# Kernel optimization log

Hardware: AMD Instinct MI355X
Metric: run time of the kernel (lower is better)

The kernel has to match this reference:

```python
import jax, jax.numpy as jnp
import numpy as np

N_GRAPHS = 256
BN_EPS = 1e-5

def gcn_conv(x, row, col, W, b, n):
    # PyG GCNConv: add self-loops, symmetric deg^-1/2 normalization, scatter-add at col.
    deg = jnp.zeros((n,), x.dtype).at[col].add(1.0) + 1.0  # +1 for self-loop
    dinv = jax.lax.rsqrt(deg)
    xw = x @ W                                             # [N, H]
    msg = (dinv[row] * dinv[col])[:, None] * xw[row]       # [E, H] gathered messages
    agg = jnp.zeros_like(xw).at[col].add(msg)              # scatter-add to targets
    agg = agg + (dinv * dinv)[:, None] * xw                # self-loop contribution
    return agg + b

def batch_norm(x, gamma, beta):
    # BatchNorm1d over the node dimension (training-mode batch statistics)
    mu = jnp.mean(x, axis=0)
    var = jnp.var(x, axis=0)
    return (x - mu) * jax.lax.rsqrt(var + BN_EPS) * gamma + beta

def setup_inputs():
    key = jax.random.key(0)
    ks = jax.random.split(key, 8)
    N, F, H, C, E = 50000, 128, 128, 3, 1_600_000
    x = jax.random.normal(ks[0], (N, F), jnp.float32)
    edge_index = jax.random.randint(ks[1], (2, E), 0, N)
    batch = jnp.sort(jax.random.randint(ks[2], (N,), 0, N_GRAPHS))
    s = lambda k, sh, fan: jax.random.normal(k, sh, jnp.float32) / np.sqrt(fan).astype(np.float32)
    return {
        "x": x, "edge_index": edge_index, "batch": batch,
        "W1": s(ks[3], (F, H), F), "b1": jnp.zeros((H,), jnp.float32),
        "gamma1": jnp.ones((H,), jnp.float32), "beta1": jnp.zeros((H,), jnp.float32),
        "W2": s(ks[4], (H, H), H), "b2": jnp.zeros((H,), jnp.float32),
        "gamma2": jnp.ones((H,), jnp.float32), "beta2": jnp.zeros((H,), jnp.float32),
        "Wc": s(ks[5], (3 * H, C), 3 * H), "bc": jnp.zeros((C,), jnp.float32),
    }

def reference(x, edge_index, batch, W1, b1, gamma1, beta1, W2, b2, gamma2, beta2, Wc, bc):
    n = x.shape[0]
    row, col = edge_index[0], edge_index[1]
    h = jax.nn.relu(batch_norm(gcn_conv(x, row, col, W1, b1, n), gamma1, beta1))
    # dropout is identity in eval mode
    h = jax.nn.relu(batch_norm(gcn_conv(h, row, col, W2, b2, n), gamma2, beta2))
    cnt = jax.ops.segment_sum(jnp.ones((n,), h.dtype), batch, num_segments=N_GRAPHS)
    hsum = jax.ops.segment_sum(h, batch, num_segments=N_GRAPHS)
    hmean = hsum / jnp.maximum(cnt, 1.0)[:, None]
    hmax = jax.ops.segment_max(h, batch, num_segments=N_GRAPHS)
    hmax = jnp.where(cnt[:, None] > 0, hmax, 0.0)  # guard empty graphs
    g = jnp.concatenate([hmean, hmax, hsum], axis=1)  # [G, 3H]
    return g @ Wc + bc
```

## Files before the change

kernel.cpp:

```cpp
#include <hip/hip_runtime.h>

#define HF 128
#define TILE 128
#define CAP2 6144
#define NFINE_MAX 512
#define SORT_CHUNK 4096
#define BN_EPS 1e-5f

__device__ __forceinline__ unsigned short f2bf(float f) {
    unsigned u = __float_as_uint(f);
    unsigned rounding = 0x7FFF + ((u >> 16) & 1);
    return (unsigned short)((u + rounding) >> 16);
}
__device__ __forceinline__ float bf2f(unsigned short u) {
    return __uint_as_float(((unsigned)u) << 16);
}
__device__ __forceinline__ unsigned packbf(float lo, float hi) {
    return ((unsigned)f2bf(hi) << 16) | (unsigned)f2bf(lo);
}

__global__ __launch_bounds__(256) void bucket_sort(const int* __restrict__ row,
                                                   const int* __restrict__ col,
                                                   unsigned* __restrict__ buckets,
                                                   int* __restrict__ cursor,
                                                   int E, int nfine) {
    __shared__ int hist[NFINE_MAX], lbase[NFINE_MAX], gbase[NFINE_MAX], lofs[NFINE_MAX];
    __shared__ int s[512];
    __shared__ unsigned staged[SORT_CHUNK];
    __shared__ unsigned short sbkt[SORT_CHUNK];
    int t = threadIdx.x;
    for (int i = t; i < NFINE_MAX; i += 256) { hist[i] = 0; lofs[i] = 0; }
    __syncthreads();
    int e0 = blockIdx.x * SORT_CHUNK;
    int n = min(SORT_CHUNK, E - e0);
    for (int i = t; i < n; i += 256) {
        int c = col[e0 + i];
        atomicAdd(&hist[c >> 7], 1);
    }
    __syncthreads();
    s[t] = hist[t];
    s[t + 256] = hist[t + 256];
    for (int o = 1; o < 512; o <<= 1) {
        __syncthreads();
        int idx = (t + 1) * (o << 1) - 1;
        if (idx < 512) s[idx] += s[idx - o];
    }
    __syncthreads();
    if (t == 0) s[511] = 0;
    for (int o = 256; o >= 1; o >>= 1) {
        __syncthreads();
        int idx = (t + 1) * (o << 1) - 1;
        if (idx < 512) { int tmp = s[idx - o]; s[idx - o] = s[idx]; s[idx] += tmp; }
    }
    __syncthreads();
    lbase[t] = s[t];
    lbase[t + 256] = s[t + 256];
    for (int b = t; b < nfine; b += 256) {
        int cnt = hist[b];
        gbase[b] = cnt ? atomicAdd(&cursor[b * 16], cnt) : 0;
    }
    __syncthreads();
    for (int i = t; i < n; i += 256) {
        int c = col[e0 + i];
        int r = row[e0 + i];
        int b = c >> 7;
        int pos = lbase[b] + atomicAdd(&lofs[b], 1);
        staged[pos] = ((unsigned)(c & 127) << 17) | (unsigned)r;
        sbkt[pos] = (unsigned short)b;
    }
    __syncthreads();
    for (int i = t; i < n; i += 256) {
        int b = sbkt[i];
        int pos = gbase[b] + (i - lbase[b]);
        if (pos < CAP2) buckets[(size_t)b * CAP2 + pos] = staged[i];
    }
}

__global__ __launch_bounds__(256) void tile_place2(const unsigned* __restrict__ buckets,
                                                   const int* __restrict__ cursor,
                                                   int* __restrict__ rowptr,
                                                   float* __restrict__ dinv,
                                                   int* __restrict__ srow,
                                                   const int* __restrict__ batch,
                                                   int* __restrict__ gstart,
                                                   int N, int NG, int nfine) {
    int b = blockIdx.x;
    int t = threadIdx.x;
    if (b < 2 && t < 129) {
        int g = b * 129 + t;
        if (g <= NG) {
            int lo = 0, hi = N;
            while (lo < hi) {
                int mid = (lo + hi) >> 1;
                if (batch[mid] < g) lo = mid + 1; else hi = mid;
            }
            gstart[g] = lo;
        }
    }
    __shared__ int h[TILE], loc[TILE], cur[TILE];
    __shared__ int red[256];
    __shared__ int stage[CAP2];
    int part = 0;
    for (int i = t; i < b; i += 256) part += min(cursor[i * 16], CAP2);
    red[t] = part;
    if (t < TILE) h[t] = 0;
    __syncthreads();
    for (int o = 128; o > 0; o >>= 1) {
        if (t < o) red[t] += red[t + o];
        __syncthreads();
    }
    int base = red[0];
    int sz = min(cursor[b * 16], CAP2);
    const unsigned* bk = buckets + (size_t)b * CAP2;
    for (int i = t; i < sz; i += 256) atomicAdd(&h[bk[i] >> 17], 1);
    __syncthreads();
    if (t < TILE) loc[t] = h[t];
    __syncthreads();
    for (int o = 1; o < TILE; o <<= 1) {
        int v = (t < TILE && t >= o) ? loc[t - o] : 0;
        __syncthreads();
        if (t < TILE) loc[t] += v;
        __syncthreads();
    }
    if (t < TILE) {
        int c = b * TILE + t;
        int excl = loc[t] - h[t];
        if (c < N) {
            rowptr[c] = base + excl;
            dinv[c] = rsqrtf((float)h[t] + 1.0f);
        }
        cur[t] = excl;
    }
    if (b == nfine - 1 && t == 0) rowptr[N] = base + sz;
    __syncthreads();
    for (int i = t; i < sz; i += 256) {
        unsigned p = bk[i];
        int pos = atomicAdd(&cur[p >> 17], 1);
        if (pos < CAP2) stage[pos] = (int)(p & 0x1FFFFu);
    }
    __syncthreads();
    for (int i = t; i < sz; i += 256) srow[base + i] = stage[i];
}

__global__ __launch_bounds__(256) void gemm_rt(const float* __restrict__ Xf,
                                               const unsigned short* __restrict__ Xh,
                                               const float* __restrict__ W,
                                               unsigned short* __restrict__ Y,
                                               const float* __restrict__ scale,
                                               const float* __restrict__ shift,
                                               const float* __restrict__ rowscale,
                                               int N, int applyBN) {
    __shared__ float xst[HF][68];
    int t = threadIdx.x;
    int row0 = blockIdx.x * 64;
    {
        int f = t & 127;
        float sc = applyBN ? scale[f] : 1.0f;
        float sh = applyBN ? shift[f] : 0.0f;
        for (int r = (t >> 7); r < 64; r += 2) {
            int rr = row0 + r;
            float v = 0.0f;
            if (rr < N) {
                if (applyBN) {
                    v = bf2f(Xh[(size_t)rr * HF + f]);
                    v = fmaxf(v * sc + sh, 0.0f);
                } else {
                    v = Xf[(size_t)rr * HF + f];
                }
            }
            xst[f][r] = v;
        }
    }
    __syncthreads();
    int cg = t & 31;
    int rg = t >> 5;
    int r0 = rg * 8;
    float acc[8][4] = {};
    const float4* Wv = reinterpret_cast<const float4*>(W);
    #pragma unroll 2
    for (int f = 0; f < HF; ++f) {
        float4 w = Wv[f * 32 + cg];
        float4 x0 = *reinterpret_cast<const float4*>(&xst[f][r0]);
        float4 x1 = *reinterpret_cast<const float4*>(&xst[f][r0 + 4]);
        float xr[8] = {x0.x, x0.y, x0.z, x0.w, x1.x, x1.y, x1.z, x1.w};
        #pragma unroll
        for (int i = 0; i < 8; ++i) {
            acc[i][0] += xr[i] * w.x;
            acc[i][1] += xr[i] * w.y;
            acc[i][2] += xr[i] * w.z;
            acc[i][3] += xr[i] * w.w;
        }
    }
    #pragma unroll
    for (int i = 0; i < 8; ++i) {
        int rr = row0 + r0 + i;
        if (rr < N) {
            float rs = rowscale[rr];
            ushort4 o;
            o.x = f2bf(acc[i][0] * rs);
            o.y = f2bf(acc[i][1] * rs);
            o.z = f2bf(acc[i][2] * rs);
            o.w = f2bf(acc[i][3] * rs);
            *reinterpret_cast<ushort4*>(&Y[(size_t)rr * HF + cg * 4]) = o;
        }
    }
}

__global__ __launch_bounds__(256) void gather_conv(const int* __restrict__ rowptr,
                                                   const int* __restrict__ srow,
                                                   const float* __restrict__ dinv,
                                                   const unsigned short* __restrict__ XW,
                                                   const float* __restrict__ b,
                                                   unsigned short* __restrict__ OUT,
                                                   float* __restrict__ psum,
                                                   float* __restrict__ psq, int N) {
    int blk = blockIdx.x;
    int c = blk * 16 + (threadIdx.x >> 4);
    int j = threadIdx.x & 15;
    bool valid = (c < N);
    const unsigned M = 0xffff0000u;
    float o[8];
    if (valid) {
        int e = rowptr[c], end = rowptr[c + 1];
        float acc[8] = {0.f, 0.f, 0.f, 0.f, 0.f, 0.f, 0.f, 0.f};
        for (; e + 3 < end; e += 4) {
            int r0 = srow[e], r1 = srow[e + 1], r2 = srow[e + 2], r3 = srow[e + 3];
            uint4 u0 = *reinterpret_cast<const uint4*>(XW + (size_t)r0 * HF + j * 8);
            uint4 u1 = *reinterpret_cast<const uint4*>(XW + (size_t)r1 * HF + j * 8);
            uint4 u2 = *reinterpret_cast<const uint4*>(XW + (size_t)r2 * HF + j * 8);
            uint4 u3 = *reinterpret_cast<const uint4*>(XW + (size_t)r3 * HF + j * 8);
            acc[0] += (__uint_as_float(u0.x << 16) + __uint_as_float(u1.x << 16))
                    + (__uint_as_float(u2.x << 16) + __uint_as_float(u3.x << 16));
            acc[1] += (__uint_as_float(u0.x & M) + __uint_as_float(u1.x & M))
                    + (__uint_as_float(u2.x & M) + __uint_as_float(u3.x & M));
            acc[2] += (__uint_as_float(u0.y << 16) + __uint_as_float(u1.y << 16))
                    + (__uint_as_float(u2.y << 16) + __uint_as_float(u3.y << 16));
            acc[3] += (__uint_as_float(u0.y & M) + __uint_as_float(u1.y & M))
                    + (__uint_as_float(u2.y & M) + __uint_as_float(u3.y & M));
            acc[4] += (__uint_as_float(u0.z << 16) + __uint_as_float(u1.z << 16))
                    + (__uint_as_float(u2.z << 16) + __uint_as_float(u3.z << 16));
            acc[5] += (__uint_as_float(u0.z & M) + __uint_as_float(u1.z & M))
                    + (__uint_as_float(u2.z & M) + __uint_as_float(u3.z & M));
            acc[6] += (__uint_as_float(u0.w << 16) + __uint_as_float(u1.w << 16))
                    + (__uint_as_float(u2.w << 16) + __uint_as_float(u3.w << 16));
            acc[7] += (__uint_as_float(u0.w & M) + __uint_as_float(u1.w & M))
                    + (__uint_as_float(u2.w & M) + __uint_as_float(u3.w & M));
        }
        for (; e < end; ++e) {
            int r0 = srow[e];
            uint4 u0 = *reinterpret_cast<const uint4*>(XW + (size_t)r0 * HF + j * 8);
            acc[0] += __uint_as_float(u0.x << 16);
            acc[1] += __uint_as_float(u0.x & M);
            acc[2] += __uint_as_float(u0.y << 16);
            acc[3] += __uint_as_float(u0.y & M);
            acc[4] += __uint_as_float(u0.z << 16);
            acc[5] += __uint_as_float(u0.z & M);
            acc[6] += __uint_as_float(u0.w << 16);
            acc[7] += __uint_as_float(u0.w & M);
        }
        float dc = dinv[c];
        uint4 xv = *reinterpret_cast<const uint4*>(XW + (size_t)c * HF + j * 8);
        acc[0] += __uint_as_float(xv.x << 16);
        acc[1] += __uint_as_float(xv.x & M);
        acc[2] += __uint_as_float(xv.y << 16);
        acc[3] += __uint_as_float(xv.y & M);
        acc[4] += __uint_as_float(xv.z << 16);
        acc[5] += __uint_as_float(xv.z & M);
        acc[6] += __uint_as_float(xv.w << 16);
        acc[7] += __uint_as_float(xv.w & M);
        float4 b0 = *reinterpret_cast<const float4*>(b + j * 8);
        float4 b1 = *reinterpret_cast<const float4*>(b + j * 8 + 4);
        float dcv = dc;
        o[0] = dcv * acc[0] + b0.x;
        o[1] = dcv * acc[1] + b0.y;
        o[2] = dcv * acc[2] + b0.z;
        o[3] = dcv * acc[3] + b0.w;
        o[4] = dcv * acc[4] + b1.x;
        o[5] = dcv * acc[5] + b1.y;
        o[6] = dcv * acc[6] + b1.z;
        o[7] = dcv * acc[7] + b1.w;
        uint4 ov;
        ov.x = packbf(o[0], o[1]);
        ov.y = packbf(o[2], o[3]);
        ov.z = packbf(o[4], o[5]);
        ov.w = packbf(o[6], o[7]);
        *reinterpret_cast<uint4*>(OUT + (size_t)c * HF + j * 8) = ov;
    } else {
        #pragma unroll
        for (int k = 0; k < 8; ++k) o[k] = 0.f;
    }
    __shared__ float sval[16][HF + 4];
    int r = threadIdx.x >> 4;
    *reinterpret_cast<float4*>(&sval[r][j * 8]) = make_float4(o[0], o[1], o[2], o[3]);
    *reinterpret_cast<float4*>(&sval[r][j * 8 + 4]) = make_float4(o[4], o[5], o[6], o[7]);
    __syncthreads();
    if (threadIdx.x < HF) {
        float s = 0.f, sq = 0.f;
        #pragma unroll
        for (int rr = 0; rr < 16; ++rr) {
            float v = sval[rr][threadIdx.x];
            s += v;
            sq += v * v;
        }
        psum[(size_t)blk * HF + threadIdx.x] = s;
        psq[(size_t)blk * HF + threadIdx.x] = sq;
    }
}

__global__ __launch_bounds__(256) void bn_reduce(const float* __restrict__ psum,
                                                 const float* __restrict__ psq,
                                                 const float* __restrict__ gamma,
                                                 const float* __restrict__ beta,
                                                 float* __restrict__ scale,
                                                 float* __restrict__ shift,
                                                 int nblk, int N) {
    int f = blockIdx.x;
    int t = threadIdx.x;
    float s = 0.f, sq = 0.f;
    for (int i = t; i < nblk; i += 256) {
        s += psum[(size_t)i * HF + f];
        sq += psq[(size_t)i * HF + f];
    }
    __shared__ float ls[256], lq[256];
    ls[t] = s; lq[t] = sq;
    __syncthreads();
    for (int o = 128; o > 0; o >>= 1) {
        if (t < o) { ls[t] += ls[t + o]; lq[t] += lq[t + o]; }
        __syncthreads();
    }
    if (t == 0) {
        float invn = 1.0f / (float)N;
        float mu = ls[0] * invn;
        float var = lq[0] * invn - mu * mu;
        float sc = gamma[f] * rsqrtf(var + BN_EPS);
        scale[f] = sc;
        shift[f] = beta[f] - mu * sc;
    }
}

__global__ __launch_bounds__(256) void pool_classify(const unsigned short* __restrict__ Bh,
                                                     const int* __restrict__ gstart,
                                                     const float* __restrict__ scale,
                                                     const float* __restrict__ shift,
                                                     const float* __restrict__ Wc,
                                                     const float* __restrict__ bc,
                                                     float* __restrict__ out) {
    int g = blockIdx.x;
    int t = threadIdx.x & 127;
    int half = threadIdx.x >> 7;
    int s0 = gstart[g], s1 = gstart[g + 1];
    float sc = scale[t], sh = shift[t];
    float sum = 0.f, mx = 0.f;
    for (int n = s0 + half; n < s1; n += 2) {
        float v = fmaxf(bf2f(Bh[(size_t)n * HF + t]) * sc + sh, 0.0f);
        sum += v;
        mx = fmaxf(mx, v);
    }
    __shared__ float shsum[2][HF], shmax[2][HF];
    __shared__ float red[3][HF];
    shsum[half][t] = sum;
    shmax[half][t] = mx;
    __syncthreads();
    if (half == 0) {
        sum += shsum[1][t];
        mx = fmaxf(mx, shmax[1][t]);
        float cntf = (float)(s1 - s0);
        float mean = sum / fmaxf(cntf, 1.0f);
        red[0][t] = mean * Wc[t * 3 + 0] + mx * Wc[(HF + t) * 3 + 0] + sum * Wc[(2 * HF + t) * 3 + 0];
        red[1][t] = mean * Wc[t * 3 + 1] + mx * Wc[(HF + t) * 3 + 1] + sum * Wc[(2 * HF + t) * 3 + 1];
        red[2][t] = mean * Wc[t * 3 + 2] + mx * Wc[(HF + t) * 3 + 2] + sum * Wc[(2 * HF + t) * 3 + 2];
    }
    __syncthreads();
    for (int o = 64; o > 0; o >>= 1) {
        if (half == 0 && t < o) {
            red[0][t] += red[0][t + o];
            red[1][t] += red[1][t + o];
            red[2][t] += red[2][t + o];
        }
        __syncthreads();
    }
    if (threadIdx.x < 3) out[g * 3 + threadIdx.x] = red[threadIdx.x][0] + bc[threadIdx.x];
}

extern "C" void kernel_launch(void* const* d_in, const int* in_sizes, int n_in,
                              void* d_out, int out_size, void* d_ws, size_t ws_size,
                              hipStream_t stream) {
    const float* x    = (const float*)d_in[0];
    const int*   ei   = (const int*)d_in[1];
    const int*   batch= (const int*)d_in[2];
    const float* W1   = (const float*)d_in[3];
    const float* b1   = (const float*)d_in[4];
    const float* g1   = (const float*)d_in[5];
    const float* be1  = (const float*)d_in[6];
    const float* W2   = (const float*)d_in[7];
    const float* b2   = (const float*)d_in[8];
    const float* g2   = (const float*)d_in[9];
    const float* be2  = (const float*)d_in[10];
    const float* Wc   = (const float*)d_in[11];
    const float* bc   = (const float*)d_in[12];
    float* out = (float*)d_out;

    const int N = in_sizes[0] / HF;
    const int E = in_sizes[1] / 2;
    const int NG = 256;
    const int* row = ei;
    const int* col = ei + E;
    const int total = N * HF;
    const int nfine = (N + TILE - 1) / TILE;
    const int nblkGa = (N + 15) / 16;

    char* w = (char*)d_ws;
    size_t off = 0;
    auto alloc = [&](size_t bytes) -> void* {
        void* p = w + off;
        off += (bytes + 255) & ~(size_t)255;
        return p;
    };
    int*            cursor    = (int*)alloc((size_t)nfine * 16 * 4);
    float*          dinv      = (float*)alloc((size_t)N * 4);
    int*            rowptr    = (int*)alloc(((size_t)N + 1) * 4);
    int*            gstart    = (int*)alloc((NG + 1) * 4);
    int*            srow      = (int*)alloc((size_t)E * 4);
    float*          psum      = (float*)alloc((size_t)nblkGa * HF * 4);
    float*          psq       = (float*)alloc((size_t)nblkGa * HF * 4);
    float*          scale     = (float*)alloc(HF * 4);
    float*          shift     = (float*)alloc(HF * 4);
    unsigned short* A         = (unsigned short*)alloc((size_t)total * 2);
    unsigned short* B         = (unsigned short*)alloc((size_t)total * 2);
    unsigned*       buckets   = (unsigned*)A;

    const int T256 = 256;
    int gridGemm = (N + 63) / 64;
    int gridSort = (E + SORT_CHUNK - 1) / SORT_CHUNK;

    hipMemsetAsync(cursor, 0, (size_t)nfine * 16 * 4, stream);
    bucket_sort<<<gridSort, T256, 0, stream>>>(row, col, buckets, cursor, E, nfine);
    tile_place2<<<nfine, T256, 0, stream>>>(buckets, cursor, rowptr, dinv, srow,
                                            batch, gstart, N, NG, nfine);

    gemm_rt<<<gridGemm, T256, 0, stream>>>(x, nullptr, W1, A, nullptr, nullptr, dinv, N, 0);
    gather_conv<<<nblkGa, T256, 0, stream>>>(rowptr, srow, dinv, A, b1, B, psum, psq, N);
    bn_reduce<<<HF, 256, 0, stream>>>(psum, psq, g1, be1, scale, shift, nblkGa, N);

    gemm_rt<<<gridGemm, T256, 0, stream>>>(nullptr, B, W2, A, scale, shift, dinv, N, 1);
    gather_conv<<<nblkGa, T256, 0, stream>>>(rowptr, srow, dinv, A, b2, B, psum, psq, N);
    bn_reduce<<<HF, 256, 0, stream>>>(psum, psq, g2, be2, scale, shift, nblkGa, N);

    pool_classify<<<NG, 256, 0, stream>>>(B, gstart, scale, shift, Wc, bc, out);
}
```

Before: 288.4 us.

## Fuse bucket sort with first GEMM in one launch, defer dinv scaling

The edge bucket sort and the first feature GEMM now run as different block ranges of a single kernel, so the two independent workloads can overlap on the GPU. Because dinv is not yet known when the GEMM runs, its row scaling moves into a separate scale_rows pass after tile_place2. The sort buckets now live in buffer B so they do not collide with the GEMM output in A. This costs an extra read-modify-write of the 50000x128 bf16 buffer and a second bf16 rounding of those values.

```diff
diff --git a/kernel.cpp b/kernel.cpp
--- a/kernel.cpp
+++ b/kernel.cpp
@@ -6,6 +6,7 @@
 #define NFINE_MAX 512
 #define SORT_CHUNK 4096
 #define BN_EPS 1e-5f
+#define SMEM_BYTES 34816
 
 __device__ __forceinline__ unsigned short f2bf(float f) {
     unsigned u = __float_as_uint(f);
@@ -19,19 +20,23 @@
     return ((unsigned)f2bf(hi) << 16) | (unsigned)f2bf(lo);
 }
 
-__global__ __launch_bounds__(256) void bucket_sort(const int* __restrict__ row,
-                                                   const int* __restrict__ col,
-                                                   unsigned* __restrict__ buckets,
-                                                   int* __restrict__ cursor,
-                                                   int E, int nfine) {
-    __shared__ int hist[NFINE_MAX], lbase[NFINE_MAX], gbase[NFINE_MAX], lofs[NFINE_MAX];
-    __shared__ int s[512];
-    __shared__ unsigned staged[SORT_CHUNK];
-    __shared__ unsigned short sbkt[SORT_CHUNK];
+__device__ __forceinline__ void bucket_sort_block(char* smem, int bid,
+                                                  const int* __restrict__ row,
+                                                  const int* __restrict__ col,
+                                                  unsigned* __restrict__ buckets,
+                                                  int* __restrict__ cursor,
+                                                  int E, int nfine) {
+    unsigned* staged = (unsigned*)smem;
+    unsigned short* sbkt = (unsigned short*)(smem + 16384);
+    int* hist  = (int*)(smem + 24576);
+    int* lbase = (int*)(smem + 26624);
+    int* gbase = (int*)(smem + 28672);
+    int* lofs  = (int*)(smem + 30720);
+    int* s     = (int*)(smem + 32768);
     int t = threadIdx.x;
     for (int i = t; i < NFINE_MAX; i += 256) { hist[i] = 0; lofs[i] = 0; }
     __syncthreads();
-    int e0 = blockIdx.x * SORT_CHUNK;
+    int e0 = bid * SORT_CHUNK;
     int n = min(SORT_CHUNK, E - e0);
     for (int i = t; i < n; i += 256) {
         int c = col[e0 + i];
@@ -74,6 +79,116 @@
         int pos = gbase[b] + (i - lbase[b]);
         if (pos < CAP2) buckets[(size_t)b * CAP2 + pos] = staged[i];
     }
+}
+
+__device__ __forceinline__ void gemm_block(char* smem, int bid,
+                                           const float* __restrict__ Xf,
+                                           const unsigned short* __restrict__ Xh,
+                                           const float* __restrict__ W,
+                                           unsigned short* __restrict__ Y,
+                                           const float* __restrict__ scale,
+                                           const float* __restrict__ shift,
+                                           const float* __restrict__ rowscale,
+                                           int N, int applyBN) {
+    float (*xst)[68] = (float(*)[68])smem;
+    int t = threadIdx.x;
+    int row0 = bid * 64;
+    {
+        int f = t & 127;
+        float sc = applyBN ? scale[f] : 1.0f;
+        float sh = applyBN ? shift[f] : 0.0f;
+        for (int r = (t >> 7); r < 64; r += 2) {
+            int rr = row0 + r;
+            float v = 0.0f;
+            if (rr < N) {
+                if (applyBN) {
+                    v = bf2f(Xh[(size_t)rr * HF + f]);
+                    v = fmaxf(v * sc + sh, 0.0f);
+                } else {
+                    v = Xf[(size_t)rr * HF + f];
+                }
+            }
+            xst[f][r] = v;
+        }
+    }
+    __syncthreads();
+    int cg = t & 31;
+    int rg = t >> 5;
+    int r0 = rg * 8;
+    float acc[8][4] = {};
+    const float4* Wv = reinterpret_cast<const float4*>(W);
+    #pragma unroll 2
+    for (int f = 0; f < HF; ++f) {
+        float4 w = Wv[f * 32 + cg];
+        float4 x0 = *reinterpret_cast<const float4*>(&xst[f][r0]);
+        float4 x1 = *reinterpret_cast<const float4*>(&xst[f][r0 + 4]);
+        float xr[8] = {x0.x, x0.y, x0.z, x0.w, x1.x, x1.y, x1.z, x1.w};
+        #pragma unroll
+        for (int i = 0; i < 8; ++i) {
+            acc[i][0] += xr[i] * w.x;
+            acc[i][1] += xr[i] * w.y;
+            acc[i][2] += xr[i] * w.z;
+            acc[i][3] += xr[i] * w.w;
+        }
+    }
+    #pragma unroll
+    for (int i = 0; i < 8; ++i) {
+        int rr = row0 + r0 + i;
+        if (rr < N) {
+            float rs = rowscale ? rowscale[rr] : 1.0f;
+            ushort4 o;
+            o.x = f2bf(acc[i][0] * rs);
+            o.y = f2bf(acc[i][1] * rs);
+            o.z = f2bf(acc[i][2] * rs);
+            o.w = f2bf(acc[i][3] * rs);
+            *reinterpret_cast<ushort4*>(&Y[(size_t)rr * HF + cg * 4]) = o;
+        }
+    }
+}
+
+__global__ __launch_bounds__(256) void sort_gemm1(const int* __restrict__ row,
+                                                  const int* __restrict__ col,
+                                                  unsigned* __restrict__ buckets,
+                                                  int* __restrict__ cursor,
+                                                  int E, int nfine, int nsort,
+                                                  const float* __restrict__ x,
+                                                  const float* __restrict__ W1,
+                                                  unsigned short* __restrict__ A,
+                                                  int N) {
+    __shared__ __align__(16) char smem[SMEM_BYTES];
+    if (blockIdx.x < nsort)
+        bucket_sort_block(smem, blockIdx.x, row, col, buckets, cursor, E, nfine);
+    else
+        gemm_block(smem, blockIdx.x - nsort, x, nullptr, W1, A,
+                   nullptr, nullptr, nullptr, N, 0);
+}
+
+__global__ __launch_bounds__(256) void gemm_rt(const unsigned short* __restrict__ Xh,
+                                               const float* __restrict__ W,
+                                               unsigned short* __restrict__ Y,
+                                               const float* __restrict__ scale,
+                                               const float* __restrict__ shift,
+                                               const float* __restrict__ rowscale,
+                                               int N) {
+    __shared__ __align__(16) char smem[SMEM_BYTES];
+    gemm_block(smem, blockIdx.x, nullptr, Xh, W, Y, scale, shift, rowscale, N, 1);
+}
+
+__global__ __launch_bounds__(256) void scale_rows(unsigned short* __restrict__ A,
+                                                  const float* __restrict__ dinv,
+                                                  int N) {
+    int idx = blockIdx.x * 256 + threadIdx.x;
+    int n = idx >> 4, j = idx & 15;
+    if (n >= N) return;
+    float dc = dinv[n];
+    const unsigned M = 0xffff0000u;
+    uint4 u = *reinterpret_cast<const uint4*>(A + (size_t)n * HF + j * 8);
+    uint4 o;
+    o.x = packbf(__uint_as_float(u.x << 16) * dc, __uint_as_float(u.x & M) * dc);
+    o.y = packbf(__uint_as_float(u.y << 16) * dc, __uint_as_float(u.y & M) * dc);
+    o.z = packbf(__uint_as_float(u.z << 16) * dc, __uint_as_float(u.z & M) * dc);
+    o.w = packbf(__uint_as_float(u.w << 16) * dc, __uint_as_float(u.w & M) * dc);
+    *reinterpret_cast<uint4*>(A + (size_t)n * HF + j * 8) = o;
 }
 
 __global__ __launch_bounds__(256) void tile_place2(const unsigned* __restrict__ buckets,
@@ -140,70 +255,6 @@
     }
     __syncthreads();
     for (int i = t; i < sz; i += 256) srow[base + i] = stage[i];
-}
-
-__global__ __launch_bounds__(256) void gemm_rt(const float* __restrict__ Xf,
-                                               const unsigned short* __restrict__ Xh,
-                                               const float* __restrict__ W,
-                                               unsigned short* __restrict__ Y,
-                                               const float* __restrict__ scale,
-                                               const float* __restrict__ shift,
-                                               const float* __restrict__ rowscale,
-                                               int N, int applyBN) {
-    __shared__ float xst[HF][68];
-    int t = threadIdx.x;
-    int row0 = blockIdx.x * 64;
-    {
-        int f = t & 127;
-        float sc = applyBN ? scale[f] : 1.0f;
-        float sh = applyBN ? shift[f] : 0.0f;
-        for (int r = (t >> 7); r < 64; r += 2) {
-            int rr = row0 + r;
-            float v = 0.0f;
-            if (rr < N) {
-                if (applyBN) {
-                    v = bf2f(Xh[(size_t)rr * HF + f]);
-                    v = fmaxf(v * sc + sh, 0.0f);
-                } else {
-                    v = Xf[(size_t)rr * HF + f];
-                }
-            }
-            xst[f][r] = v;
-        }
-    }
-    __syncthreads();
-    int cg = t & 31;
-    int rg = t >> 5;
-    int r0 = rg * 8;
-    float acc[8][4] = {};
-    const float4* Wv = reinterpret_cast<const float4*>(W);
-    #pragma unroll 2
-    for (int f = 0; f < HF; ++f) {
-        float4 w = Wv[f * 32 + cg];
-        float4 x0 = *reinterpret_cast<const float4*>(&xst[f][r0]);
-        float4 x1 = *reinterpret_cast<const float4*>(&xst[f][r0 + 4]);
-        float xr[8] = {x0.x, x0.y, x0.z, x0.w, x1.x, x1.y, x1.z, x1.w};
-        #pragma unroll
-        for (int i = 0; i < 8; ++i) {
-            acc[i][0] += xr[i] * w.x;
-            acc[i][1] += xr[i] * w.y;
-            acc[i][2] += xr[i] * w.z;
-            acc[i][3] += xr[i] * w.w;
-        }
-    }
-    #pragma unroll
-    for (int i = 0; i < 8; ++i) {
-        int rr = row0 + r0 + i;
-        if (rr < N) {
-            float rs = rowscale[rr];
-            ushort4 o;
-            o.x = f2bf(acc[i][0] * rs);
-            o.y = f2bf(acc[i][1] * rs);
-            o.z = f2bf(acc[i][2] * rs);
-            o.w = f2bf(acc[i][3] * rs);
-            *reinterpret_cast<ushort4*>(&Y[(size_t)rr * HF + cg * 4]) = o;
-        }
-    }
 }
 
 __global__ __launch_bounds__(256) void gather_conv(const int* __restrict__ rowptr,
@@ -270,15 +321,14 @@
         acc[7] += __uint_as_float(xv.w & M);
         float4 b0 = *reinterpret_cast<const float4*>(b + j * 8);
         float4 b1 = *reinterpret_cast<const float4*>(b + j * 8 + 4);
-        float dcv = dc;
-        o[0] = dcv * acc[0] + b0.x;
-        o[1] = dcv * acc[1] + b0.y;
-        o[2] = dcv * acc[2] + b0.z;
-        o[3] = dcv * acc[3] + b0.w;
-        o[4] = dcv * acc[4] + b1.x;
-        o[5] = dcv * acc[5] + b1.y;
-        o[6] = dcv * acc[6] + b1.z;
-        o[7] = dcv * acc[7] + b1.w;
+        o[0] = dc * acc[0] + b0.x;
+        o[1] = dc * acc[1] + b0.y;
+        o[2] = dc * acc[2] + b0.z;
+        o[3] = dc * acc[3] + b0.w;
+        o[4] = dc * acc[4] + b1.x;
+        o[5] = dc * acc[5] + b1.y;
+        o[6] = dc * acc[6] + b1.z;
+        o[7] = dc * acc[7] + b1.w;
         uint4 ov;
         ov.x = packbf(o[0], o[1]);
         ov.y = packbf(o[2], o[3]);
@@ -427,22 +477,24 @@
     float*          shift     = (float*)alloc(HF * 4);
     unsigned short* A         = (unsigned short*)alloc((size_t)total * 2);
     unsigned short* B         = (unsigned short*)alloc((size_t)total * 2);
-    unsigned*       buckets   = (unsigned*)A;
+    unsigned*       buckets   = (unsigned*)B;
 
     const int T256 = 256;
     int gridGemm = (N + 63) / 64;
-    int gridSort = (E + SORT_CHUNK - 1) / SORT_CHUNK;
+    int nsort    = (E + SORT_CHUNK - 1) / SORT_CHUNK;
+    int gridScl  = (N * 16 + 255) / 256;
 
     hipMemsetAsync(cursor, 0, (size_t)nfine * 16 * 4, stream);
-    bucket_sort<<<gridSort, T256, 0, stream>>>(row, col, buckets, cursor, E, nfine);
+    sort_gemm1<<<nsort + gridGemm, T256, 0, stream>>>(row, col, buckets, cursor,
+                                                      E, nfine, nsort, x, W1, A, N);
     tile_place2<<<nfine, T256, 0, stream>>>(buckets, cursor, rowptr, dinv, srow,
                                             batch, gstart, N, NG, nfine);
-
-    gemm_rt<<<gridGemm, T256, 0, stream>>>(x, nullptr, W1, A, nullptr, nullptr, dinv, N, 0);
+    scale_rows<<<gridScl, T256, 0, stream>>>(A, dinv, N);
+
     gather_conv<<<nblkGa, T256, 0, stream>>>(rowptr, srow, dinv, A, b1, B, psum, psq, N);
     bn_reduce<<<HF, 256, 0, stream>>>(psum, psq, g1, be1, scale, shift, nblkGa, N);
 
-    gemm_rt<<<gridGemm, T256, 0, stream>>>(nullptr, B, W2, A, scale, shift, dinv, N, 1);
+    gemm_rt<<<gridGemm, T256, 0, stream>>>(B, W2, A, scale, shift, dinv, N);
     gather_conv<<<nblkGa, T256, 0, stream>>>(rowptr, srow, dinv, A, b2, B, psum, psq, N);
     bn_reduce<<<HF, 256, 0, stream>>>(psum, psq, g2, be2, scale, shift, nblkGa, N);
 
```

Result: faster. 282.2 us (-2.2%).
